# Kernel tuning notes

Hardware: AMD Instinct MI355X
Metric: run time of the kernel (lower is better)

The kernel has to match this reference:

```python
import jax, jax.numpy as jnp
import numpy as np

N = 50000        # graph nodes (= GRU batch)
E = N * 32       # edges
T_ENC = 48       # encoder length
T_F = 24         # forecast_len
H = 64           # GRU hidden size (both layers)


def setup_inputs() -> dict:
    key = jax.random.key(0)
    ks = jax.random.split(key, 26)
    p = lambda i, s: jax.random.normal(ks[i], s, dtype=jnp.float32) * 0.1
    src = jax.random.randint(ks[0], (E,), 0, N, dtype=jnp.int32)
    dst = (jnp.arange(E, dtype=jnp.int32) % N)  # every node gets 32 in-edges -> bincount > 0
    return {
        "encoder_input": jax.random.normal(ks[1], (N, T_ENC, 1), dtype=jnp.float32),
        "edge_attr": jax.random.uniform(ks[2], (E,), dtype=jnp.float32, minval=0.1, maxval=1.0),
        "stat_edge_index": jnp.stack([src, dst]),
        "gru0_wih": p(3, (3 * H, 1)), "gru0_whh": p(4, (3 * H, H)),
        "gru0_bih": p(5, (3 * H,)), "gru0_bhh": p(6, (3 * H,)),
        "gru1_wih": p(7, (3 * H, H)), "gru1_whh": p(8, (3 * H, H)),
        "gru1_bih": p(9, (3 * H,)), "gru1_bhh": p(10, (3 * H,)),
        "out1_w": p(11, (H, H)), "out1_b": p(12, (H,)),
        "out2_w": p(13, (1, H)), "out2_b": p(14, (1,)),
        "gnn_w1": p(15, (64, 14)), "gnn_b1": p(16, (64,)),
        "gnn_w2": p(17, (32, 64)), "gnn_b2": p(18, (32,)),
        "gnn_wout": p(19, (1, 32)), "gnn_bout": p(20, (1,)),
        "gnn_lin_w": p(21, (1, 1)),
        "out_param": jnp.float32(0.5),
    }


def _gru_seq(x, h0, wih, whh, bih, bhh):
    """PyTorch-convention GRU over x:[N,T,in] with h0:[N,H]. Gate order r,z,n."""
    def step(h, xt):
        gi = xt @ wih.T + bih
        gh = h @ whh.T + bhh
        ir, iz, i_n = jnp.split(gi, 3, axis=-1)
        hr, hz, h_n = jnp.split(gh, 3, axis=-1)
        r = jax.nn.sigmoid(ir + hr)
        z = jax.nn.sigmoid(iz + hz)
        n = jnp.tanh(i_n + r * h_n)
        h2 = (1.0 - z) * n + z * h
        return h2, h2
    hT, ys = jax.lax.scan(step, h0, jnp.swapaxes(x, 0, 1))
    return jnp.swapaxes(ys, 0, 1), hT


def reference(encoder_input, edge_attr, stat_edge_index,
              gru0_wih, gru0_whh, gru0_bih, gru0_bhh,
              gru1_wih, gru1_whh, gru1_bih, gru1_bhh,
              out1_w, out1_b, out2_w, out2_b,
              gnn_w1, gnn_b1, gnn_w2, gnn_b2, gnn_wout, gnn_bout, gnn_lin_w,
              out_param):
    src, dst = stat_edge_index[0], stat_edge_index[1]
    grus = [(gru0_wih, gru0_whh, gru0_bih, gru0_bhh),
            (gru1_wih, gru1_whh, gru1_bih, gru1_bhh)]

    def rnn(y, hidden):
        # RNNDecoder.forward (eval: dropout = identity)
        hs = []
        for i, (wih, whh, bih, bhh) in enumerate(grus):
            h0 = hidden[i] if hidden is not None else jnp.zeros((y.shape[0], whh.shape[1]), y.dtype)
            y, hT = _gru_seq(y, h0, wih, whh, bih, bhh)
            hs.append(hT)
        out = jax.nn.relu(y @ out1_w.T + out1_b) @ out2_w.T + out2_b
        return out, hs

    # bincount(edge_index[1], weights=edge_weight)
    norm = jax.ops.segment_sum(edge_attr, dst, num_segments=N)

    def gnn(x7):
        # CustomMessagePassing: gather -> MLP(14->64->32->1) -> edge-weight scale -> scatter-add -> normalize -> lin
        x_j = x7[src]                       # [E,7]
        x_i = x7[dst]                       # [E,7]
        m = jnp.concatenate([x_j, x_j - x_i], axis=1)   # [E,14]
        m = jax.nn.relu(m @ gnn_w1.T + gnn_b1)
        m = jax.nn.relu(m @ gnn_w2.T + gnn_b2)
        m = (m @ gnn_wout.T + gnn_bout) * edge_attr[:, None]   # [E,1]
        agg = jax.ops.segment_sum(m, dst, num_segments=N)       # [N,1]
        return (agg / norm[:, None]) @ gnn_lin_w.T              # update(): lin(out/norm)

    enc_output, hidden = rnn(encoder_input, None)   # [N,T_ENC,1]
    y_prev = enc_output[:, -1, :]                   # [N,1]
    buf6 = encoder_input[:, -6:, 0]                 # [N,6] rolling history
    s = jax.nn.sigmoid(out_param)

    def dec_step(carry, _):
        buf6, y_prev, h0, h1 = carry
        x7 = jnp.concatenate([buf6, y_prev], axis=1)   # cat(step_graph_input, y_prev)[:, -7:]
        diff = gnn(x7)                                  # [N,1]
        y_seq, hs = rnn(y_prev[:, None, :], [h0, h1])   # one GRU step
        out = s * y_seq[:, 0, :] + (1.0 - s) * diff
        return (x7[:, 1:], out, hs[0], hs[1]), out

    carry = (buf6, y_prev, hidden[0], hidden[1])
    _, ys = jax.lax.scan(dec_step, carry, None, length=T_F)   # [T_F,N,1]
    decoder_output = jnp.swapaxes(ys, 0, 1)                    # [N,T_F,1]
    return decoder_output, enc_output
```

## Files before the change

kernel.cpp:

```cpp
#include <hip/hip_runtime.h>
#include <hip/hip_cooperative_groups.h>

#define NN 50000
#define TE 48
#define TF 24
#define DEG 32
#define NW 16
#define NPW 16
#define NPB 256
#define NBLK 196

#define F_W0H 0
#define F_W1I 24
#define F_W1H 48
#define F_O1W 72
#define F_GNN 80
#define DENSE_BYTES (88*1024)
#define SP64_OFF DENSE_BYTES
#define SP64_BYTES (36*64*4)
#define W2_OFF (SP64_OFF + SP64_BYTES)
#define W2_ELEM (W2_OFF/2)
#define EXTRA_OFF (W2_OFF + 4096)
#define GBUF_BYTES (EXTRA_OFF + 512)

#define L_XT_OFF EXTRA_OFF
#define L_SCR_OFF (L_XT_OFF + 512)
#define WAVE_SCR 2048
#define LDS_TOTAL (L_SCR_OFF + NW*WAVE_SCR)

typedef _Float16 f16;
typedef __attribute__((ext_vector_type(8))) _Float16 f16x8;
typedef __attribute__((ext_vector_type(2))) __fp16 fp16x2_builtin;
typedef __attribute__((ext_vector_type(4))) float f32x4;

__device__ __forceinline__ float frcp(float x) { return __builtin_amdgcn_rcpf(x); }
__device__ __forceinline__ float sigf(float x) { return frcp(1.f + __expf(-x)); }
__device__ __forceinline__ float tanhfast(float x) {
    float e = __expf(-2.f * fabsf(x));
    float r = (1.f - e) * frcp(1.f + e);
    return copysignf(r, x);
}
__device__ __forceinline__ f32x4 mf(f16x8 a, f16x8 b, f32x4 c) {
    return __builtin_amdgcn_mfma_f32_16x16x32_f16(a, b, c, 0, 0, 0);
}
__device__ __forceinline__ f16x8 ldfrag(const char* L, int f, int l) {
    return *(const f16x8*)(L + f * 1024 + l * 16);
}
__device__ __forceinline__ f16x8 spfrag64(const unsigned* sp, int tt, int l) {
    unsigned d = sp[tt * 64 + l];
    union { unsigned u; f16 h[2]; } c; c.u = d;
    f16x8 r = {};
    r[0] = c.h[0]; r[1] = c.h[1];
    return r;
}
__device__ __forceinline__ unsigned pk2(float a, float b) {
    fp16x2_builtin t = __builtin_amdgcn_cvt_pkrtz(a, b);
    union { fp16x2_builtin v; unsigned u; } c; c.v = t; return c.u;
}
__device__ __forceinline__ void upk2(unsigned u, float& a, float& b) {
    union { unsigned uu; f16 h[2]; } c; c.uu = u;
    a = (float)c.h[0]; b = (float)c.h[1];
}

struct Wctx {
    int l, g, n;
    char* S;
    const char* WL;
    const unsigned* SP;
    const float* XT;
};

__device__ __forceinline__ void transp(const Wctx& W, const uint2 (&hp)[4], f16x8 (&hB)[2]) {
    #pragma unroll
    for (int nt = 0; nt < 4; ++nt)
        *(uint2*)(W.S + W.n * 128 + (((2 * nt + (W.g >> 1)) ^ (W.n & 7)) * 16) + 8 * (W.g & 1)) = hp[nt];
    #pragma unroll
    for (int s = 0; s < 2; ++s)
        hB[s] = *(const f16x8*)(W.S + W.n * 128 + (((4 * s + W.g) ^ (W.n & 7)) * 16));
}

__device__ __forceinline__ float gru16_step(const Wctx& W, float x,
    f16x8 (&h0B)[2], f16x8 (&h1B)[2], uint2 (&h0p)[4], uint2 (&h1p)[4])
{
    const f32x4 z4 = {0.f, 0.f, 0.f, 0.f};
    const int l = W.l, g = W.g;
    f16x8 xb = {};
    if (g == 0) { xb[0] = (f16)x; xb[1] = (f16)1.0f; }

    #pragma unroll
    for (int nt = 0; nt < 4; ++nt) {
        f32x4 aR = mf(spfrag64(W.SP, nt, l), xb, z4);
        aR = mf(ldfrag(W.WL, F_W0H + nt * 2,     l), h0B[0], aR);
        aR = mf(ldfrag(W.WL, F_W0H + nt * 2 + 1, l), h0B[1], aR);
        f32x4 aZ = mf(spfrag64(W.SP, 4 + nt, l), xb, z4);
        aZ = mf(ldfrag(W.WL, F_W0H + (4 + nt) * 2,     l), h0B[0], aZ);
        aZ = mf(ldfrag(W.WL, F_W0H + (4 + nt) * 2 + 1, l), h0B[1], aZ);
        f32x4 aNi = mf(spfrag64(W.SP, 8 + nt, l), xb, z4);
        f32x4 aNh = mf(spfrag64(W.SP, 12 + nt, l), xb, z4);
        aNh = mf(ldfrag(W.WL, F_W0H + (8 + nt) * 2,     l), h0B[0], aNh);
        aNh = mf(ldfrag(W.WL, F_W0H + (8 + nt) * 2 + 1, l), h0B[1], aNh);
        float ho[4], hn[4];
        upk2(h0p[nt].x, ho[0], ho[1]);
        upk2(h0p[nt].y, ho[2], ho[3]);
        #pragma unroll
        for (int r = 0; r < 4; ++r) {
            float rg = sigf(aR[r]);
            float zg = sigf(aZ[r]);
            float ng = tanhfast(aNi[r] + rg * aNh[r]);
            hn[r] = ng + zg * (ho[r] - ng);
        }
        h0p[nt].x = pk2(hn[0], hn[1]);
        h0p[nt].y = pk2(hn[2], hn[3]);
    }
    transp(W, h0p, h0B);

    #pragma unroll
    for (int nt = 0; nt < 4; ++nt) {
        f32x4 aRa = mf(spfrag64(W.SP, 16 + nt, l), xb, z4);
        aRa = mf(ldfrag(W.WL, F_W1I + nt * 2,     l), h0B[0], aRa);
        aRa = mf(ldfrag(W.WL, F_W1I + nt * 2 + 1, l), h0B[1], aRa);
        f32x4 aRb = mf(ldfrag(W.WL, F_W1H + nt * 2, l), h1B[0], z4);
        aRb = mf(ldfrag(W.WL, F_W1H + nt * 2 + 1,   l), h1B[1], aRb);
        f32x4 aZa = mf(spfrag64(W.SP, 20 + nt, l), xb, z4);
        aZa = mf(ldfrag(W.WL, F_W1I + (4 + nt) * 2,     l), h0B[0], aZa);
        aZa = mf(ldfrag(W.WL, F_W1I + (4 + nt) * 2 + 1, l), h0B[1], aZa);
        f32x4 aZb = mf(ldfrag(W.WL, F_W1H + (4 + nt) * 2, l), h1B[0], z4);
        aZb = mf(ldfrag(W.WL, F_W1H + (4 + nt) * 2 + 1,   l), h1B[1], aZb);
        f32x4 aNi = mf(spfrag64(W.SP, 24 + nt, l), xb, z4);
        aNi = mf(ldfrag(W.WL, F_W1I + (8 + nt) * 2,     l), h0B[0], aNi);
        aNi = mf(ldfrag(W.WL, F_W1I + (8 + nt) * 2 + 1, l), h0B[1], aNi);
        f32x4 aNh = mf(spfrag64(W.SP, 28 + nt, l), xb, z4);
        aNh = mf(ldfrag(W.WL, F_W1H + (8 + nt) * 2,     l), h1B[0], aNh);
        aNh = mf(ldfrag(W.WL, F_W1H + (8 + nt) * 2 + 1, l), h1B[1], aNh);
        float ho[4], hn[4];
        upk2(h1p[nt].x, ho[0], ho[1]);
        upk2(h1p[nt].y, ho[2], ho[3]);
        #pragma unroll
        for (int r = 0; r < 4; ++r) {
            float rg = sigf(aRa[r] + aRb[r]);
            float zg = sigf(aZa[r] + aZb[r]);
            float ng = tanhfast(aNi[r] + rg * aNh[r]);
            hn[r] = ng + zg * (ho[r] - ng);
        }
        h1p[nt].x = pk2(hn[0], hn[1]);
        h1p[nt].y = pk2(hn[2], hn[3]);
    }
    transp(W, h1p, h1B);

    float y = 0.f;
    #pragma unroll
    for (int nt = 0; nt < 4; ++nt) {
        f32x4 aH = mf(spfrag64(W.SP, 32 + nt, l), xb, z4);
        aH = mf(ldfrag(W.WL, F_O1W + nt * 2,     l), h1B[0], aH);
        aH = mf(ldfrag(W.WL, F_O1W + nt * 2 + 1, l), h1B[1], aH);
        f32x4 ow = *(const f32x4*)(W.XT + 64 + nt * 16 + W.g * 4);
        #pragma unroll
        for (int r = 0; r < 4; ++r)
            y += fmaxf(aH[r], 0.f) * ow[r];
    }
    y += __shfl_xor(y, 16, 64);
    y += __shfl_xor(y, 32, 64);
    return y;
}

__device__ __forceinline__ float gru16_step_p(const Wctx& W, float x,
    uint2 (&h0p)[4], uint2 (&h1p)[4])
{
    f16x8 h0B[2], h1B[2];
    transp(W, h0p, h0B);
    transp(W, h1p, h1B);
    return gru16_step(W, x, h0B, h1B, h0p, h1p);
}

__device__ __forceinline__ void project_uv(const Wctx& W, const float (&win)[7],
    bool valid, int node, char* __restrict__ ubw, float (&vf)[16])
{
    const f32x4 z4 = {0.f, 0.f, 0.f, 0.f};
    const int g = W.g, n = W.n;
    f16x8 xw = {};
    if (g == 0) {
        #pragma unroll
        for (int j = 0; j < 7; ++j) xw[j] = (f16)win[j];
        xw[7] = (f16)1.0f;
    }
    #pragma unroll
    for (int mt = 0; mt < 4; ++mt) {
        f32x4 a = mf(ldfrag(W.WL, F_GNN + mt, W.l), xw, z4);
        uint2 wv; wv.x = pk2(a[0], a[1]); wv.y = pk2(a[2], a[3]);
        *(uint2*)(W.S + n * 128 + ((mt ^ (n & 3)) * 32) + g * 8) = wv;
    }
    {
        f16x8 uu0 = *(const f16x8*)(W.S + n * 128 + ((((g >> 1))     ^ (n & 3)) * 32) + (g & 1) * 16);
        f16x8 uu1 = *(const f16x8*)(W.S + n * 128 + (((2 + (g >> 1)) ^ (n & 3)) * 32) + (g & 1) * 16);
        int w0 = __builtin_amdgcn_cvt_pk_fp8_f32((float)uu0[0], (float)uu0[1], 0, false);
        w0     = __builtin_amdgcn_cvt_pk_fp8_f32((float)uu0[2], (float)uu0[3], w0, true);
        int w1 = __builtin_amdgcn_cvt_pk_fp8_f32((float)uu0[4], (float)uu0[5], 0, false);
        w1     = __builtin_amdgcn_cvt_pk_fp8_f32((float)uu0[6], (float)uu0[7], w1, true);
        int w2 = __builtin_amdgcn_cvt_pk_fp8_f32((float)uu1[0], (float)uu1[1], 0, false);
        w2     = __builtin_amdgcn_cvt_pk_fp8_f32((float)uu1[2], (float)uu1[3], w2, true);
        int w3 = __builtin_amdgcn_cvt_pk_fp8_f32((float)uu1[4], (float)uu1[5], 0, false);
        w3     = __builtin_amdgcn_cvt_pk_fp8_f32((float)uu1[6], (float)uu1[7], w3, true);
        uint4 pk;
        pk.x = (unsigned)w0; pk.y = (unsigned)w1; pk.z = (unsigned)w2; pk.w = (unsigned)w3;
        if (valid) *(uint4*)(ubw + (size_t)node * 64 + g * 16) = pk;
    }
    #pragma unroll
    for (int mt = 0; mt < 4; ++mt) {
        f32x4 a = mf(ldfrag(W.WL, F_GNN + 4 + mt, W.l), xw, z4);
        uint2 wv; wv.x = pk2(a[0], a[1]); wv.y = pk2(a[2], a[3]);
        *(uint2*)(W.S + n * 128 + ((mt ^ (n & 3)) * 32) + g * 8) = wv;
    }
    {
        f16x8 v0 = *(const f16x8*)(W.S + n * 128 + ((((g >> 1))     ^ (n & 3)) * 32) + (g & 1) * 16);
        f16x8 v1 = *(const f16x8*)(W.S + n * 128 + (((2 + (g >> 1)) ^ (n & 3)) * 32) + (g & 1) * 16);
        #pragma unroll
        for (int e = 0; e < 8; ++e) {
            vf[e]     = (float)v0[e];
            vf[8 + e] = (float)v1[e];
        }
    }
}

__device__ __forceinline__ void stage_all(char* smem, const f16* wfrag, int tid) {
    uint4* d = (uint4*)smem;
    const uint4* s4 = (const uint4*)wfrag;
    for (int i = tid; i < EXTRA_OFF / 16; i += 1024) d[i] = s4[i];
    if (tid < 32) {
        uint4* de = (uint4*)(smem + L_XT_OFF);
        const uint4* se = (const uint4*)((const char*)wfrag + EXTRA_OFF);
        de[tid] = se[tid];
    }
    __syncthreads();
}

__global__ __launch_bounds__(256)
void pack_weights(const float* __restrict__ w0i, const float* __restrict__ w0h,
                  const float* __restrict__ b0i, const float* __restrict__ b0h,
                  const float* __restrict__ w1i, const float* __restrict__ w1h,
                  const float* __restrict__ b1i, const float* __restrict__ b1h,
                  const float* __restrict__ o1w, const float* __restrict__ o1b,
                  const float* __restrict__ gw1, const float* __restrict__ gb1,
                  const float* __restrict__ gw2, const float* __restrict__ gb2,
                  const float* __restrict__ gwo, const float* __restrict__ o2w,
                  f16* __restrict__ wf)
{
    const int i = blockIdx.x * 256 + threadIdx.x;
    if (i < 92 * 64) {
        const int f = i >> 6, l = i & 63;
        const int lr = l & 15, g = l >> 4;
        f16x8 out = {};
        if (f < F_GNN) {
            const float* src; int fb;
            if (f < F_W1I)      { src = w0h; fb = f; }
            else if (f < F_W1H) { src = w1i; fb = f - F_W1I; }
            else if (f < F_O1W) { src = w1h; fb = f - F_W1H; }
            else                { src = o1w; fb = f - F_O1W; }
            const int nt = fb >> 1, s = fb & 1;
            const int row = nt * 16 + lr, k0 = s * 32 + g * 8;
            #pragma unroll
            for (int e = 0; e < 8; ++e) out[e] = (f16)src[row * 64 + k0 + e];
            *(f16x8*)&wf[f * 512 + l * 8] = out;
        } else if (f < 88) {
            const int mt = f - F_GNN;
            const int m = mt * 16 + lr;
            #pragma unroll
            for (int e = 0; e < 8; ++e) {
                int k = g * 8 + e; float v = 0.f;
                if (m < 64) {
                    if (k < 7) v = gw1[m * 14 + k] + gw1[m * 14 + 7 + k];
                    else if (k == 7) v = gb1[m];
                } else {
                    int mm = m - 64;
                    if (k < 7) v = -gw1[mm * 14 + 7 + k];
                }
                out[e] = (f16)v;
            }
            *(f16x8*)&wf[f * 512 + l * 8] = out;
        } else {
            const int fb = f - 88, nt = fb >> 1, s = fb & 1;
            const int row = nt * 16 + lr, k0 = s * 32 + g * 8;
            #pragma unroll
            for (int e = 0; e < 8; ++e) out[e] = (f16)gw2[row * 64 + k0 + e];
            *(f16x8*)&wf[W2_ELEM + fb * 512 + l * 8] = out;
        }
    } else if (i < 92 * 64 + 36 * 64) {
        const int e = i - 92 * 64;
        const int tt = e >> 6, l = e & 63;
        unsigned val = 0u;
        if (l < 16) {
            const int r16 = l;
            float c0 = 0.f, c1 = 0.f;
            if (tt < 8)       { int row = tt*16 + r16;            c0 = w0i[row]; c1 = b0i[row] + b0h[row]; }
            else if (tt < 12) { int row = 128 + (tt-8)*16 + r16;  c0 = w0i[row]; c1 = b0i[row]; }
            else if (tt < 16) { int row = 128 + (tt-12)*16 + r16; c1 = b0h[row]; }
            else if (tt < 24) { int row = (tt-16)*16 + r16;       c1 = b1i[row] + b1h[row]; }
            else if (tt < 28) { int row = 128 + (tt-24)*16 + r16; c1 = b1i[row]; }
            else if (tt < 32) { int row = 128 + (tt-28)*16 + r16; c1 = b1h[row]; }
            else              { int row = (tt-32)*16 + r16;       c1 = o1b[row]; }
            fp16x2_builtin t = __builtin_amdgcn_cvt_pkrtz(c0, c1);
            union { fp16x2_builtin v; unsigned u; } c; c.v = t;
            val = c.u;
        }
        ((unsigned*)((char*)wf + SP64_OFF))[tt * 64 + l] = val;
    } else if (i < 92 * 64 + 36 * 64 + 128) {
        const int idx = i - 92 * 64 - 36 * 64;
        float v;
        if (idx < 32) v = gb2[idx];
        else if (idx < 64) v = gwo[idx - 32];
        else v = o2w[idx - 64];
        float* xf = (float*)((char*)wf + EXTRA_OFF);
        xf[idx] = v;
    }
}

__global__ __launch_bounds__(1024, 4)
void enc_kernel(const float* __restrict__ enc_in, const float* __restrict__ o2b,
                const f16* __restrict__ wfrag, float* __restrict__ enc_out,
                uint2* __restrict__ hsb, float* __restrict__ hist,
                char* __restrict__ ub0)
{
    extern __shared__ char smem[];
    const int tid = threadIdx.x;
    stage_all(smem, wfrag, tid);

    Wctx W;
    W.l = tid & 63;
    const int wid = __builtin_amdgcn_readfirstlane(tid >> 6);
    W.g = W.l >> 4; W.n = W.l & 15;
    W.WL = smem;
    W.SP = (const unsigned*)(smem + SP64_OFF);
    W.XT = (const float*)(smem + L_XT_OFF);
    W.S  = smem + L_SCR_OFF + wid * WAVE_SCR;

    const int node = blockIdx.x * NPB + wid * NPW + W.n;
    const bool valid = node < NN;
    const int ndc = valid ? node : NN - 1;
    const float o2b0 = o2b[0];

    f16x8 h0B[2] = {}, h1B[2] = {};
    uint2 h0p[4] = {}, h1p[4] = {};
    const float* pe = enc_in + (size_t)ndc * TE;
    float y = 0.f;
    for (int t = 0; t < TE; ++t) {
        y = gru16_step(W, pe[t], h0B, h1B, h0p, h1p) + o2b0;
        if (W.g == 0 && valid) enc_out[(size_t)node * TE + t] = y;
    }
    {
        uint2* hb0 = hsb + ((size_t)ndc * 2 + 0) * 16 + W.g * 4;
        uint2* hb1 = hsb + ((size_t)ndc * 2 + 1) * 16 + W.g * 4;
        uint4 a0 = {h0p[0].x, h0p[0].y, h0p[1].x, h0p[1].y};
        uint4 a1 = {h0p[2].x, h0p[2].y, h0p[3].x, h0p[3].y};
        uint4 b0 = {h1p[0].x, h1p[0].y, h1p[1].x, h1p[1].y};
        uint4 b1 = {h1p[2].x, h1p[2].y, h1p[3].x, h1p[3].y};
        if (valid) {
            *(uint4*)&hb0[0] = a0; *(uint4*)&hb0[2] = a1;
            *(uint4*)&hb1[0] = b0; *(uint4*)&hb1[2] = b1;
        }
    }
    float win[7];
    #pragma unroll
    for (int j = 0; j < 6; ++j) win[j] = pe[42 + j];
    win[6] = y;
    if (W.g == 0 && valid) {
        #pragma unroll
        for (int j = 0; j < 7; ++j) hist[(size_t)node * 8 + j] = win[j];
    }
    float vf[16];
    project_uv(W, win, valid, node, ub0, vf);
}

__global__ __launch_bounds__(1024, 3)
void dec_kernel(const int* __restrict__ eidx, const float* __restrict__ ea,
                const float* __restrict__ o2b, const float* __restrict__ oparam,
                const float* __restrict__ lin_w, const float* __restrict__ bo,
                const f16* __restrict__ wfrag, float* __restrict__ dec_out,
                const uint2* __restrict__ hsb, const float* __restrict__ hist,
                char* __restrict__ ub0, char* __restrict__ ub1)
{
    extern __shared__ char smem[];
    const int tid = threadIdx.x;
    stage_all(smem, wfrag, tid);

    Wctx W;
    W.l = tid & 63;
    const int wid = __builtin_amdgcn_readfirstlane(tid >> 6);
    W.g = W.l >> 4; W.n = W.l & 15;
    W.WL = smem;
    W.SP = (const unsigned*)(smem + SP64_OFF);
    W.XT = (const float*)(smem + L_XT_OFF);
    W.S  = smem + L_SCR_OFF + wid * WAVE_SCR;

    const f32x4 z4 = {0.f, 0.f, 0.f, 0.f};
    const int g = W.g;
    const int node = blockIdx.x * NPB + wid * NPW + W.n;
    const bool valid = node < NN;
    const int ndc = valid ? node : NN - 1;

    const float o2b0 = o2b[0];
    const float sv = sigf(oparam[0]);
    const float bo0 = bo[0];

    float eav[DEG];
    int srcoff[DEG];
    #pragma unroll
    for (int k = 0; k < DEG; ++k) {
        eav[k] = ea[(size_t)k * NN + ndc];
        srcoff[k] = eidx[(size_t)k * NN + ndc] * 64 + g * 16;
    }
    float invc, nb0;
    {
        float nr = 0.f;
        #pragma unroll
        for (int k = 0; k < DEG; ++k) nr += (g == (k >> 3)) ? eav[k] : 0.f;
        nr = 0.f;
        #pragma unroll
        for (int kk = 0; kk < 8; ++kk) nr += ea[(size_t)(g * 8 + kk) * NN + ndc];
        nr += __shfl_xor(nr, 16, 64);
        nr += __shfl_xor(nr, 32, 64);
        invc = (1.f - sv) * lin_w[0] * frcp(nr);
        nb0 = bo0 * nr;
    }

    uint2 h0p[4], h1p[4];
    {
        const uint2* hb0 = hsb + ((size_t)ndc * 2 + 0) * 16 + g * 4;
        const uint2* hb1 = hsb + ((size_t)ndc * 2 + 1) * 16 + g * 4;
        #pragma unroll
        for (int nt = 0; nt < 4; ++nt) { h0p[nt] = hb0[nt]; h1p[nt] = hb1[nt]; }
    }

    float win[7];
    #pragma unroll
    for (int j = 0; j < 7; ++j) win[j] = (g == 0) ? hist[(size_t)ndc * 8 + j] : 0.f;

    float vf[16];
    project_uv(W, win, valid, node, ub0, vf);

    for (int t = 0; t < TF; ++t) {
        cooperative_groups::this_grid().sync();
        const char* ub = (t & 1) ? ub1 : ub0;
        char*      ubw = (t & 1) ? ub0 : ub1;

        f16x8 Aw2[2][2];
        #pragma unroll
        for (int nj = 0; nj < 2; ++nj)
            #pragma unroll
            for (int s = 0; s < 2; ++s)
                Aw2[nj][s] = *(const f16x8*)(smem + W2_OFF + (nj * 2 + s) * 1024 + W.l * 16);
        f32x4 b2r0 = *(const f32x4*)(W.XT + 0  + g * 4);
        f32x4 b2r1 = *(const f32x4*)(W.XT + 16 + g * 4);
        f32x4 wor0 = *(const f32x4*)(W.XT + 32 + g * 4);
        f32x4 wor1 = *(const f32x4*)(W.XT + 48 + g * 4);

        float S = 0.f;
        #pragma unroll
        for (int k = 0; k < DEG; ++k) {
            uint4 U = *(const uint4*)(ub + srcoff[k]);
            unsigned wd[4];
            wd[0] = U.x; wd[1] = U.y; wd[2] = U.z; wd[3] = U.w;
            unsigned mw[8];
            #pragma unroll
            for (int c = 0; c < 4; ++c) {
                auto a = __builtin_amdgcn_cvt_pk_f32_fp8((int)wd[c], false);
                auto b = __builtin_amdgcn_cvt_pk_f32_fp8((int)wd[c], true);
                float e0 = fmaxf(a[0] + vf[c * 4 + 0], 0.f);
                float e1 = fmaxf(a[1] + vf[c * 4 + 1], 0.f);
                float e2 = fmaxf(b[0] + vf[c * 4 + 2], 0.f);
                float e3 = fmaxf(b[1] + vf[c * 4 + 3], 0.f);
                mw[c * 2]     = pk2(e0, e1);
                mw[c * 2 + 1] = pk2(e2, e3);
            }
            union { uint4 u; f16x8 h; } M0, M1;
            M0.u.x = mw[0]; M0.u.y = mw[1]; M0.u.z = mw[2]; M0.u.w = mw[3];
            M1.u.x = mw[4]; M1.u.y = mw[5]; M1.u.z = mw[6]; M1.u.w = mw[7];
            f32x4 acc0 = mf(Aw2[0][0], M0.h, z4); acc0 = mf(Aw2[0][1], M1.h, acc0);
            f32x4 acc1 = mf(Aw2[1][0], M0.h, z4); acc1 = mf(Aw2[1][1], M1.h, acc1);
            float ps = 0.f;
            #pragma unroll
            for (int r = 0; r < 4; ++r)
                ps += fmaxf(acc0[r] + b2r0[r], 0.f) * wor0[r]
                    + fmaxf(acc1[r] + b2r1[r], 0.f) * wor1[r];
            S = fmaf(ps, eav[k], S);
        }
        S += __shfl_xor(S, 16, 64);
        S += __shfl_xor(S, 32, 64);
        const float aggT = S + nb0;

        float y = gru16_step_p(W, win[6], h0p, h1p) + o2b0;
        float o = sv * y + aggT * invc;
        if (g == 0 && valid) dec_out[(size_t)node * TF + t] = o;
        #pragma unroll
        for (int j = 0; j < 6; ++j) win[j] = win[j + 1];
        win[6] = o;
        if (t < TF - 1) project_uv(W, win, valid, node, ubw, vf);
    }
}

extern "C" void kernel_launch(void* const* d_in, const int* in_sizes, int n_in,
                              void* d_out, int out_size, void* d_ws, size_t ws_size,
                              hipStream_t stream)
{
    const float* enc_in = (const float*)d_in[0];
    const float* ea     = (const float*)d_in[1];
    const int*   eidx   = (const int*)d_in[2];
    const float* w0i = (const float*)d_in[3];
    const float* w0h = (const float*)d_in[4];
    const float* b0i = (const float*)d_in[5];
    const float* b0h = (const float*)d_in[6];
    const float* w1i = (const float*)d_in[7];
    const float* w1h = (const float*)d_in[8];
    const float* b1i = (const float*)d_in[9];
    const float* b1h = (const float*)d_in[10];
    const float* o1w = (const float*)d_in[11];
    const float* o1b = (const float*)d_in[12];
    const float* o2w = (const float*)d_in[13];
    const float* o2b = (const float*)d_in[14];
    const float* gw1  = (const float*)d_in[15];
    const float* gb1  = (const float*)d_in[16];
    const float* gw2  = (const float*)d_in[17];
    const float* gb2  = (const float*)d_in[18];
    const float* gwo  = (const float*)d_in[19];
    const float* gbo  = (const float*)d_in[20];
    const float* glin = (const float*)d_in[21];
    const float* gop  = (const float*)d_in[22];

    float* dec_out = (float*)d_out;
    float* enc_out = dec_out + (size_t)NN * TF;

    char* ws = (char*)d_ws;
    f16* wfrag = (f16*)ws;
    char* p = ws + ((GBUF_BYTES + 255) & ~255);
    char*  ub0  = p;          p += (size_t)NN * 64;
    char*  ub1  = p;          p += (size_t)NN * 64;
    uint2* hsb  = (uint2*)p;  p += (size_t)NN * 32 * 8;
    float* hist = (float*)p;  p += (size_t)NN * 8 * 4;

    (void)hipFuncSetAttribute((const void*)enc_kernel,
        hipFuncAttributeMaxDynamicSharedMemorySize, LDS_TOTAL);
    (void)hipFuncSetAttribute((const void*)dec_kernel,
        hipFuncAttributeMaxDynamicSharedMemorySize, LDS_TOTAL);

    pack_weights<<<33, 256, 0, stream>>>(w0i, w0h, b0i, b0h, w1i, w1h, b1i, b1h,
                                         o1w, o1b, gw1, gb1, gw2, gb2, gwo, o2w, wfrag);

    enc_kernel<<<NBLK, 1024, LDS_TOTAL, stream>>>(enc_in, o2b, wfrag, enc_out,
                                                  hsb, hist, ub0);

    void* args[] = {
        (void*)&eidx, (void*)&ea, (void*)&o2b, (void*)&gop, (void*)&glin, (void*)&gbo,
        (void*)&wfrag, (void*)&dec_out, (void*)&hsb, (void*)&hist,
        (void*)&ub0, (void*)&ub1
    };
    (void)hipLaunchCooperativeKernel((const void*)dec_kernel, dim3(NBLK), dim3(1024),
                                     args, LDS_TOTAL, stream);
}
```

Measured before the change: 2.267 ms.

## Interleave GRU decoder step with software-pipelined GNN edge gathers

Splits the GRU step into layer-0, layer-1 halves and head, and interleaves them with the 32-edge GNN gather loop. The gathers are issued eight at a time through inline global_load_dwordx4 into double buffers, with explicit vmcnt waits and sched barriers, so memory latency hides behind the GRU MFMA work. It also lowers the launch-bounds occupancy hint from 3 to 2 blocks per CU so the extra buffer registers fit. It also removes a redundant re-read of edge attributes for the norm. The costs are lower occupancy and hand-set waitcnt ordering that the compiler cannot check.

```diff
diff --git a/kernel.cpp b/kernel.cpp
--- a/kernel.cpp
+++ b/kernel.cpp
@@ -79,14 +79,11 @@
         hB[s] = *(const f16x8*)(W.S + W.n * 128 + (((4 * s + W.g) ^ (W.n & 7)) * 16));
 }
 
-__device__ __forceinline__ float gru16_step(const Wctx& W, float x,
-    f16x8 (&h0B)[2], f16x8 (&h1B)[2], uint2 (&h0p)[4], uint2 (&h1p)[4])
+__device__ __forceinline__ void gru_l0(const Wctx& W, f16x8 xb,
+    const f16x8 (&h0B)[2], uint2 (&h0p)[4])
 {
     const f32x4 z4 = {0.f, 0.f, 0.f, 0.f};
-    const int l = W.l, g = W.g;
-    f16x8 xb = {};
-    if (g == 0) { xb[0] = (f16)x; xb[1] = (f16)1.0f; }
-
+    const int l = W.l;
     #pragma unroll
     for (int nt = 0; nt < 4; ++nt) {
         f32x4 aR = mf(spfrag64(W.SP, nt, l), xb, z4);
@@ -112,10 +109,16 @@
         h0p[nt].x = pk2(hn[0], hn[1]);
         h0p[nt].y = pk2(hn[2], hn[3]);
     }
-    transp(W, h0p, h0B);
-
-    #pragma unroll
-    for (int nt = 0; nt < 4; ++nt) {
+}
+
+template<int NT0, int NT1>
+__device__ __forceinline__ void gru_l1(const Wctx& W, f16x8 xb,
+    const f16x8 (&h0B)[2], const f16x8 (&h1B)[2], uint2 (&h1p)[4])
+{
+    const f32x4 z4 = {0.f, 0.f, 0.f, 0.f};
+    const int l = W.l;
+    #pragma unroll
+    for (int nt = NT0; nt < NT1; ++nt) {
         f32x4 aRa = mf(spfrag64(W.SP, 16 + nt, l), xb, z4);
         aRa = mf(ldfrag(W.WL, F_W1I + nt * 2,     l), h0B[0], aRa);
         aRa = mf(ldfrag(W.WL, F_W1I + nt * 2 + 1, l), h0B[1], aRa);
@@ -145,8 +148,12 @@
         h1p[nt].x = pk2(hn[0], hn[1]);
         h1p[nt].y = pk2(hn[2], hn[3]);
     }
-    transp(W, h1p, h1B);
-
+}
+
+__device__ __forceinline__ float gru_head(const Wctx& W, f16x8 xb, const f16x8 (&h1B)[2])
+{
+    const f32x4 z4 = {0.f, 0.f, 0.f, 0.f};
+    const int l = W.l;
     float y = 0.f;
     #pragma unroll
     for (int nt = 0; nt < 4; ++nt) {
@@ -163,13 +170,16 @@
     return y;
 }
 
-__device__ __forceinline__ float gru16_step_p(const Wctx& W, float x,
-    uint2 (&h0p)[4], uint2 (&h1p)[4])
-{
-    f16x8 h0B[2], h1B[2];
+__device__ __forceinline__ float gru16_step(const Wctx& W, float x,
+    f16x8 (&h0B)[2], f16x8 (&h1B)[2], uint2 (&h0p)[4], uint2 (&h1p)[4])
+{
+    f16x8 xb = {};
+    if (W.g == 0) { xb[0] = (f16)x; xb[1] = (f16)1.0f; }
+    gru_l0(W, xb, h0B, h0p);
     transp(W, h0p, h0B);
+    gru_l1<0, 4>(W, xb, h0B, h1B, h1p);
     transp(W, h1p, h1B);
-    return gru16_step(W, x, h0B, h1B, h0p, h1p);
+    return gru_head(W, xb, h1B);
 }
 
 __device__ __forceinline__ void project_uv(const Wctx& W, const float (&win)[7],
@@ -369,7 +379,7 @@
     project_uv(W, win, valid, node, ub0, vf);
 }
 
-__global__ __launch_bounds__(1024, 3)
+__global__ __launch_bounds__(1024, 2)
 void dec_kernel(const int* __restrict__ eidx, const float* __restrict__ ea,
                 const float* __restrict__ o2b, const float* __restrict__ oparam,
                 const float* __restrict__ lin_w, const float* __restrict__ bo,
@@ -411,10 +421,7 @@
     {
         float nr = 0.f;
         #pragma unroll
-        for (int k = 0; k < DEG; ++k) nr += (g == (k >> 3)) ? eav[k] : 0.f;
-        nr = 0.f;
-        #pragma unroll
-        for (int kk = 0; kk < 8; ++kk) nr += ea[(size_t)(g * 8 + kk) * NN + ndc];
+        for (int kk = 0; kk < 8; ++kk) nr += eav[g * 8 + kk];
         nr += __shfl_xor(nr, 16, 64);
         nr += __shfl_xor(nr, 32, 64);
         invc = (1.f - sv) * lin_w[0] * frcp(nr);
@@ -453,40 +460,80 @@
         f32x4 wor1 = *(const f32x4*)(W.XT + 48 + g * 4);
 
         float S = 0.f;
-        #pragma unroll
-        for (int k = 0; k < DEG; ++k) {
-            uint4 U = *(const uint4*)(ub + srcoff[k]);
-            unsigned wd[4];
-            wd[0] = U.x; wd[1] = U.y; wd[2] = U.z; wd[3] = U.w;
-            unsigned mw[8];
+        uint4 UA[8], UB[8];
+
+        auto issue8 = [&](uint4 (&U)[8], int kb) {
             #pragma unroll
-            for (int c = 0; c < 4; ++c) {
-                auto a = __builtin_amdgcn_cvt_pk_f32_fp8((int)wd[c], false);
-                auto b = __builtin_amdgcn_cvt_pk_f32_fp8((int)wd[c], true);
-                float e0 = fmaxf(a[0] + vf[c * 4 + 0], 0.f);
-                float e1 = fmaxf(a[1] + vf[c * 4 + 1], 0.f);
-                float e2 = fmaxf(b[0] + vf[c * 4 + 2], 0.f);
-                float e3 = fmaxf(b[1] + vf[c * 4 + 3], 0.f);
-                mw[c * 2]     = pk2(e0, e1);
-                mw[c * 2 + 1] = pk2(e2, e3);
+            for (int k = 0; k < 8; ++k) {
+                const char* up = ub + srcoff[kb * 8 + k];
+                asm volatile("global_load_dwordx4 %0, %1, off"
+                             : "=&v"(U[k]) : "v"(up) : "memory");
             }
-            union { uint4 u; f16x8 h; } M0, M1;
-            M0.u.x = mw[0]; M0.u.y = mw[1]; M0.u.z = mw[2]; M0.u.w = mw[3];
-            M1.u.x = mw[4]; M1.u.y = mw[5]; M1.u.z = mw[6]; M1.u.w = mw[7];
-            f32x4 acc0 = mf(Aw2[0][0], M0.h, z4); acc0 = mf(Aw2[0][1], M1.h, acc0);
-            f32x4 acc1 = mf(Aw2[1][0], M0.h, z4); acc1 = mf(Aw2[1][1], M1.h, acc1);
-            float ps = 0.f;
+        };
+        auto mlp8 = [&](const uint4 (&U)[8], int kb) {
             #pragma unroll
-            for (int r = 0; r < 4; ++r)
-                ps += fmaxf(acc0[r] + b2r0[r], 0.f) * wor0[r]
-                    + fmaxf(acc1[r] + b2r1[r], 0.f) * wor1[r];
-            S = fmaf(ps, eav[k], S);
-        }
+            for (int k = 0; k < 8; ++k) {
+                unsigned wd[4];
+                wd[0] = U[k].x; wd[1] = U[k].y; wd[2] = U[k].z; wd[3] = U[k].w;
+                unsigned mw[8];
+                #pragma unroll
+                for (int c = 0; c < 4; ++c) {
+                    auto a = __builtin_amdgcn_cvt_pk_f32_fp8((int)wd[c], false);
+                    auto b = __builtin_amdgcn_cvt_pk_f32_fp8((int)wd[c], true);
+                    float e0 = fmaxf(a[0] + vf[c * 4 + 0], 0.f);
+                    float e1 = fmaxf(a[1] + vf[c * 4 + 1], 0.f);
+                    float e2 = fmaxf(b[0] + vf[c * 4 + 2], 0.f);
+                    float e3 = fmaxf(b[1] + vf[c * 4 + 3], 0.f);
+                    mw[c * 2]     = pk2(e0, e1);
+                    mw[c * 2 + 1] = pk2(e2, e3);
+                }
+                union { uint4 u; f16x8 h; } M0, M1;
+                M0.u.x = mw[0]; M0.u.y = mw[1]; M0.u.z = mw[2]; M0.u.w = mw[3];
+                M1.u.x = mw[4]; M1.u.y = mw[5]; M1.u.z = mw[6]; M1.u.w = mw[7];
+                f32x4 acc0 = mf(Aw2[0][0], M0.h, z4); acc0 = mf(Aw2[0][1], M1.h, acc0);
+                f32x4 acc1 = mf(Aw2[1][0], M0.h, z4); acc1 = mf(Aw2[1][1], M1.h, acc1);
+                float ps = 0.f;
+                #pragma unroll
+                for (int r = 0; r < 4; ++r)
+                    ps += fmaxf(acc0[r] + b2r0[r], 0.f) * wor0[r]
+                        + fmaxf(acc1[r] + b2r1[r], 0.f) * wor1[r];
+                S = fmaf(ps, eav[kb * 8 + k], S);
+            }
+        };
+
+        f16x8 xb = {};
+        if (g == 0) { xb[0] = (f16)win[6]; xb[1] = (f16)1.0f; }
+        f16x8 h0B[2], h1B[2];
+        transp(W, h0p, h0B);
+        transp(W, h1p, h1B);
+
+        issue8(UA, 0);
+        gru_l0(W, xb, h0B, h0p);
+        transp(W, h0p, h0B);
+        issue8(UB, 1);
+        asm volatile("s_waitcnt vmcnt(8)" ::: "memory");
+        __builtin_amdgcn_sched_barrier(0);
+        mlp8(UA, 0);
+        gru_l1<0, 2>(W, xb, h0B, h1B, h1p);
+        issue8(UA, 2);
+        asm volatile("s_waitcnt vmcnt(8)" ::: "memory");
+        __builtin_amdgcn_sched_barrier(0);
+        mlp8(UB, 1);
+        gru_l1<2, 4>(W, xb, h0B, h1B, h1p);
+        issue8(UB, 3);
+        asm volatile("s_waitcnt vmcnt(8)" ::: "memory");
+        __builtin_amdgcn_sched_barrier(0);
+        mlp8(UA, 2);
+        transp(W, h1p, h1B);
+        float y = gru_head(W, xb, h1B) + o2b0;
+        asm volatile("s_waitcnt vmcnt(0)" ::: "memory");
+        __builtin_amdgcn_sched_barrier(0);
+        mlp8(UB, 3);
+
         S += __shfl_xor(S, 16, 64);
         S += __shfl_xor(S, 32, 64);
         const float aggT = S + nb0;
 
-        float y = gru16_step_p(W, win[6], h0p, h1p) + o2b0;
         float o = sv * y + aggT * invc;
         if (g == 0 && valid) dec_out[(size_t)node * TF + t] = o;
         #pragma unroll
```

Result: slower. 2.878 ms (+26.9%).

## Gather raw fp16 source windows and recompute first GNN layer per edge via MFMA

Applied to the files above, without the earlier changes.

Each node now publishes only its 7-value history window in fp16 (16 bytes) instead of precomputed fp8 first-layer projections (64 bytes). The decoder gathers that window per edge and recomputes the first GNN layer with an MFMA that combines source and destination operands, cutting gather traffic and removing the fp8 quantization. The cost is extra MFMA and LDS work per edge. The gather is software-pipelined two edges ahead, and the decoder launch bound rises from 3 to 4 blocks per CU.

```diff
diff --git a/kernel.cpp b/kernel.cpp
--- a/kernel.cpp
+++ b/kernel.cpp
@@ -79,14 +79,11 @@
         hB[s] = *(const f16x8*)(W.S + W.n * 128 + (((4 * s + W.g) ^ (W.n & 7)) * 16));
 }
 
-__device__ __forceinline__ float gru16_step(const Wctx& W, float x,
-    f16x8 (&h0B)[2], f16x8 (&h1B)[2], uint2 (&h0p)[4], uint2 (&h1p)[4])
+__device__ __forceinline__ void gru_l0(const Wctx& W, f16x8 xb,
+    const f16x8 (&h0B)[2], uint2 (&h0p)[4])
 {
     const f32x4 z4 = {0.f, 0.f, 0.f, 0.f};
-    const int l = W.l, g = W.g;
-    f16x8 xb = {};
-    if (g == 0) { xb[0] = (f16)x; xb[1] = (f16)1.0f; }
-
+    const int l = W.l;
     #pragma unroll
     for (int nt = 0; nt < 4; ++nt) {
         f32x4 aR = mf(spfrag64(W.SP, nt, l), xb, z4);
@@ -112,10 +109,16 @@
         h0p[nt].x = pk2(hn[0], hn[1]);
         h0p[nt].y = pk2(hn[2], hn[3]);
     }
-    transp(W, h0p, h0B);
-
-    #pragma unroll
-    for (int nt = 0; nt < 4; ++nt) {
+}
+
+template<int NT0, int NT1>
+__device__ __forceinline__ void gru_l1(const Wctx& W, f16x8 xb,
+    const f16x8 (&h0B)[2], const f16x8 (&h1B)[2], uint2 (&h1p)[4])
+{
+    const f32x4 z4 = {0.f, 0.f, 0.f, 0.f};
+    const int l = W.l;
+    #pragma unroll
+    for (int nt = NT0; nt < NT1; ++nt) {
         f32x4 aRa = mf(spfrag64(W.SP, 16 + nt, l), xb, z4);
         aRa = mf(ldfrag(W.WL, F_W1I + nt * 2,     l), h0B[0], aRa);
         aRa = mf(ldfrag(W.WL, F_W1I + nt * 2 + 1, l), h0B[1], aRa);
@@ -145,8 +148,12 @@
         h1p[nt].x = pk2(hn[0], hn[1]);
         h1p[nt].y = pk2(hn[2], hn[3]);
     }
-    transp(W, h1p, h1B);
-
+}
+
+__device__ __forceinline__ float gru_head(const Wctx& W, f16x8 xb, const f16x8 (&h1B)[2])
+{
+    const f32x4 z4 = {0.f, 0.f, 0.f, 0.f};
+    const int l = W.l;
     float y = 0.f;
     #pragma unroll
     for (int nt = 0; nt < 4; ++nt) {
@@ -163,6 +170,18 @@
     return y;
 }
 
+__device__ __forceinline__ float gru16_step(const Wctx& W, float x,
+    f16x8 (&h0B)[2], f16x8 (&h1B)[2], uint2 (&h0p)[4], uint2 (&h1p)[4])
+{
+    f16x8 xb = {};
+    if (W.g == 0) { xb[0] = (f16)x; xb[1] = (f16)1.0f; }
+    gru_l0(W, xb, h0B, h0p);
+    transp(W, h0p, h0B);
+    gru_l1<0, 4>(W, xb, h0B, h1B, h1p);
+    transp(W, h1p, h1B);
+    return gru_head(W, xb, h1B);
+}
+
 __device__ __forceinline__ float gru16_step_p(const Wctx& W, float x,
     uint2 (&h0p)[4], uint2 (&h1p)[4])
 {
@@ -170,55 +189,6 @@
     transp(W, h0p, h0B);
     transp(W, h1p, h1B);
     return gru16_step(W, x, h0B, h1B, h0p, h1p);
-}
-
-__device__ __forceinline__ void project_uv(const Wctx& W, const float (&win)[7],
-    bool valid, int node, char* __restrict__ ubw, float (&vf)[16])
-{
-    const f32x4 z4 = {0.f, 0.f, 0.f, 0.f};
-    const int g = W.g, n = W.n;
-    f16x8 xw = {};
-    if (g == 0) {
-        #pragma unroll
-        for (int j = 0; j < 7; ++j) xw[j] = (f16)win[j];
-        xw[7] = (f16)1.0f;
-    }
-    #pragma unroll
-    for (int mt = 0; mt < 4; ++mt) {
-        f32x4 a = mf(ldfrag(W.WL, F_GNN + mt, W.l), xw, z4);
-        uint2 wv; wv.x = pk2(a[0], a[1]); wv.y = pk2(a[2], a[3]);
-        *(uint2*)(W.S + n * 128 + ((mt ^ (n & 3)) * 32) + g * 8) = wv;
-    }
-    {
-        f16x8 uu0 = *(const f16x8*)(W.S + n * 128 + ((((g >> 1))     ^ (n & 3)) * 32) + (g & 1) * 16);
-        f16x8 uu1 = *(const f16x8*)(W.S + n * 128 + (((2 + (g >> 1)) ^ (n & 3)) * 32) + (g & 1) * 16);
-        int w0 = __builtin_amdgcn_cvt_pk_fp8_f32((float)uu0[0], (float)uu0[1], 0, false);
-        w0     = __builtin_amdgcn_cvt_pk_fp8_f32((float)uu0[2], (float)uu0[3], w0, true);
-        int w1 = __builtin_amdgcn_cvt_pk_fp8_f32((float)uu0[4], (float)uu0[5], 0, false);
-        w1     = __builtin_amdgcn_cvt_pk_fp8_f32((float)uu0[6], (float)uu0[7], w1, true);
-        int w2 = __builtin_amdgcn_cvt_pk_fp8_f32((float)uu1[0], (float)uu1[1], 0, false);
-        w2     = __builtin_amdgcn_cvt_pk_fp8_f32((float)uu1[2], (float)uu1[3], w2, true);
-        int w3 = __builtin_amdgcn_cvt_pk_fp8_f32((float)uu1[4], (float)uu1[5], 0, false);
-        w3     = __builtin_amdgcn_cvt_pk_fp8_f32((float)uu1[6], (float)uu1[7], w3, true);
-        uint4 pk;
-        pk.x = (unsigned)w0; pk.y = (unsigned)w1; pk.z = (unsigned)w2; pk.w = (unsigned)w3;
-        if (valid) *(uint4*)(ubw + (size_t)node * 64 + g * 16) = pk;
-    }
-    #pragma unroll
-    for (int mt = 0; mt < 4; ++mt) {
-        f32x4 a = mf(ldfrag(W.WL, F_GNN + 4 + mt, W.l), xw, z4);
-        uint2 wv; wv.x = pk2(a[0], a[1]); wv.y = pk2(a[2], a[3]);
-        *(uint2*)(W.S + n * 128 + ((mt ^ (n & 3)) * 32) + g * 8) = wv;
-    }
-    {
-        f16x8 v0 = *(const f16x8*)(W.S + n * 128 + ((((g >> 1))     ^ (n & 3)) * 32) + (g & 1) * 16);
-        f16x8 v1 = *(const f16x8*)(W.S + n * 128 + (((2 + (g >> 1)) ^ (n & 3)) * 32) + (g & 1) * 16);
-        #pragma unroll
-        for (int e = 0; e < 8; ++e) {
-            vf[e]     = (float)v0[e];
-            vf[8 + e] = (float)v1[e];
-        }
-    }
 }
 
 __device__ __forceinline__ void stage_all(char* smem, const f16* wfrag, int tid) {
@@ -262,18 +232,22 @@
             *(f16x8*)&wf[f * 512 + l * 8] = out;
         } else if (f < 88) {
             const int mt = f - F_GNN;
-            const int m = mt * 16 + lr;
-            #pragma unroll
-            for (int e = 0; e < 8; ++e) {
-                int k = g * 8 + e; float v = 0.f;
-                if (m < 64) {
-                    if (k < 7) v = gw1[m * 14 + k] + gw1[m * 14 + 7 + k];
-                    else if (k == 7) v = gb1[m];
-                } else {
-                    int mm = m - 64;
-                    if (k < 7) v = -gw1[mm * 14 + 7 + k];
+            if (mt < 4) {
+                const int row = mt * 16 + lr;
+                if (g == 0) {
+                    #pragma unroll
+                    for (int e = 0; e < 8; ++e) {
+                        float v = (e < 7) ? (gw1[row * 14 + e] + gw1[row * 14 + 7 + e])
+                                          : gb1[row];
+                        out[e] = (f16)v;
+                    }
+                } else if (g == 1) {
+                    #pragma unroll
+                    for (int e = 0; e < 8; ++e) {
+                        float v = (e < 7) ? -gw1[row * 14 + 7 + e] : 0.f;
+                        out[e] = (f16)v;
+                    }
                 }
-                out[e] = (f16)v;
             }
             *(f16x8*)&wf[f * 512 + l * 8] = out;
         } else {
@@ -317,7 +291,7 @@
 void enc_kernel(const float* __restrict__ enc_in, const float* __restrict__ o2b,
                 const f16* __restrict__ wfrag, float* __restrict__ enc_out,
                 uint2* __restrict__ hsb, float* __restrict__ hist,
-                char* __restrict__ ub0)
+                f16* __restrict__ xw0)
 {
     extern __shared__ char smem[];
     const int tid = threadIdx.x;
@@ -364,18 +338,21 @@
     if (W.g == 0 && valid) {
         #pragma unroll
         for (int j = 0; j < 7; ++j) hist[(size_t)node * 8 + j] = win[j];
-    }
-    float vf[16];
-    project_uv(W, win, valid, node, ub0, vf);
-}
-
-__global__ __launch_bounds__(1024, 3)
+        f16x8 xwv = {};
+        #pragma unroll
+        for (int j = 0; j < 7; ++j) xwv[j] = (f16)win[j];
+        xwv[7] = (f16)1.0f;
+        *(f16x8*)&xw0[(size_t)node * 8] = xwv;
+    }
+}
+
+__global__ __launch_bounds__(1024, 4)
 void dec_kernel(const int* __restrict__ eidx, const float* __restrict__ ea,
                 const float* __restrict__ o2b, const float* __restrict__ oparam,
                 const float* __restrict__ lin_w, const float* __restrict__ bo,
                 const f16* __restrict__ wfrag, float* __restrict__ dec_out,
                 const uint2* __restrict__ hsb, const float* __restrict__ hist,
-                char* __restrict__ ub0, char* __restrict__ ub1)
+                f16* __restrict__ xw0, f16* __restrict__ xw1)
 {
     extern __shared__ char smem[];
     const int tid = threadIdx.x;
@@ -391,8 +368,8 @@
     W.S  = smem + L_SCR_OFF + wid * WAVE_SCR;
 
     const f32x4 z4 = {0.f, 0.f, 0.f, 0.f};
-    const int g = W.g;
-    const int node = blockIdx.x * NPB + wid * NPW + W.n;
+    const int g = W.g, n = W.n;
+    const int node = blockIdx.x * NPB + wid * NPW + n;
     const bool valid = node < NN;
     const int ndc = valid ? node : NN - 1;
 
@@ -405,16 +382,13 @@
     #pragma unroll
     for (int k = 0; k < DEG; ++k) {
         eav[k] = ea[(size_t)k * NN + ndc];
-        srcoff[k] = eidx[(size_t)k * NN + ndc] * 64 + g * 16;
+        srcoff[k] = eidx[(size_t)k * NN + ndc] * 16;
     }
     float invc, nb0;
     {
         float nr = 0.f;
         #pragma unroll
-        for (int k = 0; k < DEG; ++k) nr += (g == (k >> 3)) ? eav[k] : 0.f;
-        nr = 0.f;
-        #pragma unroll
-        for (int kk = 0; kk < 8; ++kk) nr += ea[(size_t)(g * 8 + kk) * NN + ndc];
+        for (int kk = 0; kk < 8; ++kk) nr += eav[g * 8 + kk];
         nr += __shfl_xor(nr, 16, 64);
         nr += __shfl_xor(nr, 32, 64);
         invc = (1.f - sv) * lin_w[0] * frcp(nr);
@@ -431,15 +405,12 @@
 
     float win[7];
     #pragma unroll
-    for (int j = 0; j < 7; ++j) win[j] = (g == 0) ? hist[(size_t)ndc * 8 + j] : 0.f;
-
-    float vf[16];
-    project_uv(W, win, valid, node, ub0, vf);
+    for (int j = 0; j < 7; ++j) win[j] = hist[(size_t)ndc * 8 + j];
 
     for (int t = 0; t < TF; ++t) {
         cooperative_groups::this_grid().sync();
-        const char* ub = (t & 1) ? ub1 : ub0;
-        char*      ubw = (t & 1) ? ub0 : ub1;
+        const char* xwc = (const char*)((t & 1) ? xw1 : xw0);
+        f16*        xwn = (t & 1) ? xw0 : xw1;
 
         f16x8 Aw2[2][2];
         #pragma unroll
@@ -452,35 +423,49 @@
         f32x4 wor0 = *(const f32x4*)(W.XT + 32 + g * 4);
         f32x4 wor1 = *(const f32x4*)(W.XT + 48 + g * 4);
 
+        f16x8 xdst = {};
+        if (g == 1) {
+            #pragma unroll
+            for (int j = 0; j < 7; ++j) xdst[j] = (f16)win[j];
+            xdst[7] = (f16)1.0f;
+        }
+
         float S = 0.f;
-        #pragma unroll
-        for (int k = 0; k < DEG; ++k) {
-            uint4 U = *(const uint4*)(ub + srcoff[k]);
-            unsigned wd[4];
-            wd[0] = U.x; wd[1] = U.y; wd[2] = U.z; wd[3] = U.w;
-            unsigned mw[8];
-            #pragma unroll
-            for (int c = 0; c < 4; ++c) {
-                auto a = __builtin_amdgcn_cvt_pk_f32_fp8((int)wd[c], false);
-                auto b = __builtin_amdgcn_cvt_pk_f32_fp8((int)wd[c], true);
-                float e0 = fmaxf(a[0] + vf[c * 4 + 0], 0.f);
-                float e1 = fmaxf(a[1] + vf[c * 4 + 1], 0.f);
-                float e2 = fmaxf(b[0] + vf[c * 4 + 2], 0.f);
-                float e3 = fmaxf(b[1] + vf[c * 4 + 3], 0.f);
-                mw[c * 2]     = pk2(e0, e1);
-                mw[c * 2 + 1] = pk2(e2, e3);
+        auto body = [&](int k, f16x8 xs) {
+            f16x8 bfrag = (g == 0) ? xs : xdst;
+            #pragma unroll
+            for (int mt = 0; mt < 4; ++mt) {
+                f32x4 mm = mf(ldfrag(W.WL, F_GNN + mt, W.l), bfrag, z4);
+                uint2 wv;
+                wv.x = pk2(fmaxf(mm[0], 0.f), fmaxf(mm[1], 0.f));
+                wv.y = pk2(fmaxf(mm[2], 0.f), fmaxf(mm[3], 0.f));
+                *(uint2*)(W.S + n * 128 + ((mt ^ (n & 3)) * 32) + g * 8) = wv;
             }
-            union { uint4 u; f16x8 h; } M0, M1;
-            M0.u.x = mw[0]; M0.u.y = mw[1]; M0.u.z = mw[2]; M0.u.w = mw[3];
-            M1.u.x = mw[4]; M1.u.y = mw[5]; M1.u.z = mw[6]; M1.u.w = mw[7];
-            f32x4 acc0 = mf(Aw2[0][0], M0.h, z4); acc0 = mf(Aw2[0][1], M1.h, acc0);
-            f32x4 acc1 = mf(Aw2[1][0], M0.h, z4); acc1 = mf(Aw2[1][1], M1.h, acc1);
+            f16x8 B0 = *(const f16x8*)(W.S + n * 128 + ((((g >> 1))     ^ (n & 3)) * 32) + (g & 1) * 16);
+            f16x8 B1 = *(const f16x8*)(W.S + n * 128 + (((2 + (g >> 1)) ^ (n & 3)) * 32) + (g & 1) * 16);
+            f32x4 acc0 = mf(Aw2[0][0], B0, z4); acc0 = mf(Aw2[0][1], B1, acc0);
+            f32x4 acc1 = mf(Aw2[1][0], B0, z4); acc1 = mf(Aw2[1][1], B1, acc1);
             float ps = 0.f;
             #pragma unroll
             for (int r = 0; r < 4; ++r)
                 ps += fmaxf(acc0[r] + b2r0[r], 0.f) * wor0[r]
                     + fmaxf(acc1[r] + b2r1[r], 0.f) * wor1[r];
             S = fmaf(ps, eav[k], S);
+        };
+
+        f16x8 xsA = {}, xsB = {};
+        if (g == 0) {
+            xsA = *(const f16x8*)(xwc + srcoff[0]);
+            xsB = *(const f16x8*)(xwc + srcoff[1]);
+        }
+        #pragma unroll
+        for (int kb = 0; kb < 16; ++kb) {
+            f16x8 nA = {}, nB = {};
+            if (g == 0 && 2 * kb + 2 < DEG) nA = *(const f16x8*)(xwc + srcoff[2 * kb + 2]);
+            if (g == 0 && 2 * kb + 3 < DEG) nB = *(const f16x8*)(xwc + srcoff[2 * kb + 3]);
+            body(2 * kb,     xsA);
+            body(2 * kb + 1, xsB);
+            xsA = nA; xsB = nB;
         }
         S += __shfl_xor(S, 16, 64);
         S += __shfl_xor(S, 32, 64);
@@ -492,7 +477,13 @@
         #pragma unroll
         for (int j = 0; j < 6; ++j) win[j] = win[j + 1];
         win[6] = o;
-        if (t < TF - 1) project_uv(W, win, valid, node, ubw, vf);
+        if (t < TF - 1 && g == 0 && valid) {
+            f16x8 xwv = {};
+            #pragma unroll
+            for (int j = 0; j < 7; ++j) xwv[j] = (f16)win[j];
+            xwv[7] = (f16)1.0f;
+            *(f16x8*)&xwn[(size_t)node * 8] = xwv;
+        }
     }
 }
 
@@ -530,8 +521,8 @@
     char* ws = (char*)d_ws;
     f16* wfrag = (f16*)ws;
     char* p = ws + ((GBUF_BYTES + 255) & ~255);
-    char*  ub0  = p;          p += (size_t)NN * 64;
-    char*  ub1  = p;          p += (size_t)NN * 64;
+    f16*   xw0  = (f16*)p;    p += (size_t)NN * 8 * 2;
+    f16*   xw1  = (f16*)p;    p += (size_t)NN * 8 * 2;
     uint2* hsb  = (uint2*)p;  p += (size_t)NN * 32 * 8;
     float* hist = (float*)p;  p += (size_t)NN * 8 * 4;
 
@@ -544,12 +535,12 @@
                                          o1w, o1b, gw1, gb1, gw2, gb2, gwo, o2w, wfrag);
 
     enc_kernel<<<NBLK, 1024, LDS_TOTAL, stream>>>(enc_in, o2b, wfrag, enc_out,
-                                                  hsb, hist, ub0);
+                                                  hsb, hist, xw0);
 
     void* args[] = {
         (void*)&eidx, (void*)&ea, (void*)&o2b, (void*)&gop, (void*)&glin, (void*)&gbo,
         (void*)&wfrag, (void*)&dec_out, (void*)&hsb, (void*)&hist,
-        (void*)&ub0, (void*)&ub1
+        (void*)&xw0, (void*)&xw1
     };
     (void)hipLaunchCooperativeKernel((const void*)dec_kernel, dim3(NBLK), dim3(1024),
                                      args, LDS_TOTAL, stream);
```

New measurement: 3.739 ms. 1.65x slower.
